# Performance work log

Hardware: AMD Instinct MI355X
Metric: run time of the kernel (lower is better)

## Reference

```python
import jax, jax.numpy as jnp
import numpy as np

B, S, DIM, HEADS, HEAD_DIM = 2, 1536, 1024, 16, 64
BLOCK_SIZE, LOOK_AHEAD, LOOK_BACKWARD = 24, 1, 1
ROPE_THETA = 10000.0


def setup_inputs() -> dict:
    key = jax.random.key(0)
    ks = jax.random.split(key, 6)
    s = 0.02  # init scale for weights
    return {
        "x": jax.random.normal(ks[0], (B, S, DIM), jnp.float32),
        "Wq": jax.random.normal(ks[1], (DIM, DIM), jnp.float32) * s,
        "bq": jnp.zeros((DIM,), jnp.float32),
        "Wk": jax.random.normal(ks[2], (DIM, DIM), jnp.float32) * s,
        "bk": jnp.zeros((DIM,), jnp.float32),
        "Wv": jax.random.normal(ks[3], (DIM, DIM), jnp.float32) * s,
        "bv": jnp.zeros((DIM,), jnp.float32),
        "Wo": jax.random.normal(ks[4], (DIM, DIM), jnp.float32) * s,
        "bo": jnp.zeros((DIM,), jnp.float32),
        "position_ids": jnp.arange(S, dtype=jnp.int32),
    }


def _rotate_half(v):
    # pairs (x1, x2) -> (-x2, x1), interleaved (matches torch reshape/unbind/stack)
    v2 = v.reshape(*v.shape[:-1], -1, 2)
    x1, x2 = v2[..., 0], v2[..., 1]
    return jnp.stack((-x2, x1), axis=-1).reshape(v.shape)


def _rope_tables(position_ids):
    # DitRotary: theta_i = 1/ROPE_THETA^(2i/rotary_dim), i=0..31; cos/sin duplicated
    # pairwise -> [c0,c0,c1,c1,...] of length HEAD_DIM
    inv_freq = 1.0 / (ROPE_THETA ** (jnp.arange(0, HEAD_DIM, 2, dtype=jnp.float32) / HEAD_DIM))
    ang = position_ids.astype(jnp.float32)[:, None] * inv_freq[None, :]  # [S, 32]
    cos = jnp.repeat(jnp.cos(ang), 2, axis=-1)  # [S, HEAD_DIM]
    sin = jnp.repeat(jnp.sin(ang), 2, axis=-1)
    return cos, sin


def reference(x, Wq, bq, Wk, bk, Wv, bv, Wo, bo, position_ids):
    b, s, _ = x.shape
    q = (x @ Wq + bq).reshape(b, s, HEADS, HEAD_DIM)
    k = (x @ Wk + bk).reshape(b, s, HEADS, HEAD_DIM)
    v = (x @ Wv + bv).reshape(b, s, HEADS, HEAD_DIM)

    # Partial rotary: applied ONLY to head 0 (torch slices dim=2 == heads)
    cos, sin = _rope_tables(position_ids)            # [S, HEAD_DIM]
    q0 = q[:, :, 0, :] * cos + _rotate_half(q[:, :, 0, :]) * sin
    k0 = k[:, :, 0, :] * cos + _rotate_half(k[:, :, 0, :]) * sin
    q = jnp.concatenate([q0[:, :, None, :], q[:, :, 1:, :]], axis=2)
    k = jnp.concatenate([k0[:, :, None, :], k[:, :, 1:, :]], axis=2)

    # Block-banded mask: diff[i, j] = block(j) - block(i)
    blk = position_ids // BLOCK_SIZE
    diff = blk[None, :] - blk[:, None]               # [S, S]
    allowed = (diff >= -LOOK_BACKWARD) & (diff <= LOOK_AHEAD)
    neg = jnp.where(allowed, 0.0, jnp.finfo(jnp.float32).min)  # ~mask * finfo.min

    scale = 1.0 / jnp.sqrt(jnp.float32(HEAD_DIM))
    scores = jnp.einsum("bqhd,bkhd->bhqk", q, k) * scale + neg[None, None]
    attn = jax.nn.softmax(scores.astype(jnp.float32), axis=-1).astype(q.dtype)
    out = jnp.einsum("bhqk,bkhd->bqhd", attn, v).reshape(b, s, HEADS * HEAD_DIM)
    return out @ Wo + bo
```

## Files before the change

kernel.cpp:

```cpp
#include <hip/hip_runtime.h>
#include <hip/hip_bf16.h>
#include <stdint.h>

typedef _Float16 f16;
typedef _Float16 f16x8 __attribute__((ext_vector_type(8)));
typedef float    f32x4 __attribute__((ext_vector_type(4)));
typedef unsigned short u16;
typedef unsigned int   u32;

#define S_LEN 1536
#define NDIM  1024
#define MROWS 3072

__device__ __forceinline__ u16 f2h(float f){
  _Float16 h = (_Float16)f;
  return __builtin_bit_cast(u16, h);
}

#define GLDS16(g, l) __builtin_amdgcn_global_load_lds( \
    (const __attribute__((address_space(1))) u32*)(const void*)(g), \
    (__attribute__((address_space(3))) u32*)(void*)(l), 16, 0, 0)

__global__ __launch_bounds__(256) void cast_f32_f16(
    const float* __restrict__ in, u16* __restrict__ out)
{
  const int i = blockIdx.x * 256 + threadIdx.x;
  const float4* p = (const float4*)in;
  float4 a = p[i*2], b = p[i*2+1];
  alignas(16) u16 tmp[8];
  tmp[0]=f2h(a.x); tmp[1]=f2h(a.y); tmp[2]=f2h(a.z); tmp[3]=f2h(a.w);
  tmp[4]=f2h(b.x); tmp[5]=f2h(b.y); tmp[6]=f2h(b.z); tmp[7]=f2h(b.w);
  *(uint4*)(out + (size_t)i*8) = *(const uint4*)tmp;
}

__global__ __launch_bounds__(256) void transpose4(
    const float* __restrict__ w0, const float* __restrict__ w1,
    const float* __restrict__ w2, const float* __restrict__ w3,
    u16* __restrict__ out)
{
  const float* W = (blockIdx.z==0)?w0:(blockIdx.z==1)?w1:(blockIdx.z==2)?w2:w3;
  u16* O = out + (size_t)blockIdx.z * (1024u*1024u);
  __shared__ __align__(16) u16 T[64*72];
  const int t = threadIdx.x;
  const int r0 = blockIdx.y*64, c0 = blockIdx.x*64;
  #pragma unroll
  for (int i=0;i<2;i++){
    int v = t + i*256;
    int row = v >> 3, col = (v & 7) * 8;
    const float* src = W + (size_t)(r0+row)*NDIM + c0 + col;
    float4 a = *(const float4*)src;
    float4 b = *(const float4*)(src + 4);
    alignas(16) u16 tmp[8];
    tmp[0]=f2h(a.x); tmp[1]=f2h(a.y); tmp[2]=f2h(a.z); tmp[3]=f2h(a.w);
    tmp[4]=f2h(b.x); tmp[5]=f2h(b.y); tmp[6]=f2h(b.z); tmp[7]=f2h(b.w);
    *(uint4*)(T + row*72 + col) = *(const uint4*)tmp;
  }
  __syncthreads();
  #pragma unroll
  for (int i=0;i<2;i++){
    int v = t + i*256;
    int cc = v >> 3, rr = (v & 7) * 8;
    alignas(16) u16 tmp[8];
    #pragma unroll
    for (int j=0;j<8;j++) tmp[j] = T[(rr+j)*72 + cc];
    *(uint4*)(O + (size_t)(c0+cc)*NDIM + r0 + rr) = *(const uint4*)tmp;
  }
}

#define SUBK 32

__global__ __launch_bounds__(256) void gemm_bias_rope(
    const u16* __restrict__ A,
    const u16* __restrict__ BT,
    const float* __restrict__ b0, const float* __restrict__ b1,
    const float* __restrict__ b2,
    u16*   __restrict__ Ch,
    float* __restrict__ Cf,
    const int* __restrict__ pos,
    int M, int rope_mats, int f32_out)
{
  __shared__ __align__(16) u16 As[2*128*SUBK];
  __shared__ __align__(16) u16 Bs[2*64*SUBK];

  const int t    = threadIdx.x;
  const int lane = t & 63;
  const int wave = t >> 6;
  const int z    = blockIdx.z;
  const int m0   = blockIdx.y * 128;
  const int n0   = blockIdx.x * 64;
  const u16* Bm  = BT + (size_t)z * (1024u*1024u);
  u16*       Cm  = Ch ? (Ch + (size_t)z * ((size_t)M * NDIM)) : (u16*)0;
  const float* bias = (z==0) ? b0 : ((z==1) ? b1 : b2);

  const int wm   = (wave >> 1) * 64;
  const int wn   = (wave & 1) * 32;
  const int l15  = lane & 15;
  const int quad = lane >> 4;

  const int lrow = lane >> 2;
  const int lcol = (lane & 3) * 8;
  const u16* gA = A  + (size_t)(m0 + wave*32 + lrow)*NDIM + lcol;
  const u16* gB = Bm + (size_t)(n0 + wave*16 + lrow)*NDIM + lcol;
  u16* lA = As + (wave*32)*SUBK;
  u16* lB = Bs + (wave*16)*SUBK;

  f32x4 acc[4][2];
  #pragma unroll
  for (int i=0;i<4;i++)
    #pragma unroll
    for (int j=0;j<2;j++)
      acc[i][j] = (f32x4){0.f,0.f,0.f,0.f};

  for (int k0 = 0; k0 < 1024; k0 += 64) {
    #pragma unroll
    for (int kb=0;kb<2;kb++){
      const u16* ga = gA + k0 + kb*SUBK;
      u16* la = lA + kb*(128*SUBK);
      GLDS16(ga,           la);
      GLDS16(ga + 16*NDIM, la + 16*SUBK);
      GLDS16(gB + k0 + kb*SUBK, lB + kb*(64*SUBK));
    }
    __syncthreads();
    #pragma unroll
    for (int kb=0;kb<2;kb++){
      f16x8 af[4], bfr[2];
      #pragma unroll
      for (int i=0;i<4;i++)
        af[i]  = *(const f16x8*)(As + kb*(128*SUBK) + (wm + i*16 + l15)*SUBK + quad*8);
      #pragma unroll
      for (int j=0;j<2;j++)
        bfr[j] = *(const f16x8*)(Bs + kb*(64*SUBK)  + (wn + j*16 + l15)*SUBK + quad*8);
      #pragma unroll
      for (int i=0;i<4;i++)
        #pragma unroll
        for (int j=0;j<2;j++)
          acc[i][j] = __builtin_amdgcn_mfma_f32_16x16x32_f16(
                          af[i], bfr[j], acc[i][j], 0, 0, 0);
    }
    __syncthreads();
  }

  const bool rope_tile = (z < rope_mats) && (n0 == 0);
  #pragma unroll
  for (int i=0;i<4;i++){
    const int rbase = m0 + wm + i*16 + quad*4;
    #pragma unroll
    for (int j=0;j<2;j++){
      const int c  = n0 + wn + j*16 + l15;
      const float bv = bias[c];
      f32x4 v4 = acc[i][j];
      #pragma unroll
      for (int r=0;r<4;r++) v4[r] += bv;
      if (rope_tile) {
        const int   ii  = c >> 1;
        const float inv = powf(10000.0f, -(float)ii * (1.0f/32.0f));
        const float sgn = (c & 1) ? 1.0f : -1.0f;
        #pragma unroll
        for (int r=0;r<4;r++){
          float val     = v4[r];
          float partner = __shfl_xor(val, 1, 64);
          int   srow    = (rbase + r) % S_LEN;
          float ang     = (float)pos[srow] * inv;
          float sv, cv;
          sincosf(ang, &sv, &cv);
          v4[r] = val * cv + sgn * partner * sv;
        }
      }
      if (f32_out) {
        #pragma unroll
        for (int r=0;r<4;r++)
          Cf[(size_t)(rbase + r)*NDIM + c] = v4[r];
      } else {
        #pragma unroll
        for (int r=0;r<4;r++)
          Cm[(size_t)(rbase + r)*NDIM + c] = f2h(v4[r]);
      }
    }
  }
}

__global__ __launch_bounds__(256) void attn_kernel(
    const u16* __restrict__ q, const u16* __restrict__ k,
    const u16* __restrict__ v, u16* __restrict__ o)
{
  const int qb = blockIdx.x;
  const int h  = blockIdx.y;
  const int b  = blockIdx.z;
  const int t  = threadIdx.x;
  const int lane = t & 63;
  const int wave = t >> 6;
  const int l15  = lane & 15;
  const int quad = lane >> 4;

  const int ks_ = (qb == 0) ? 0 : (qb - 1) * 24;
  const int ke_ = min(S_LEN, (qb + 2) * 24);
  const int kn  = ke_ - ks_;

  __shared__ __align__(16) u16   Qs[32*72];
  __shared__ __align__(16) u16   Ks[80*72];
  __shared__ __align__(16) u16   Vt[64*104];
  __shared__ __align__(16) float Ss[32*80];
  __shared__ __align__(16) u16   Ps[32*104];

  const size_t qrow0 = (size_t)b*S_LEN + qb*24;
  const size_t krow0 = (size_t)b*S_LEN + ks_;
  const int hoff = h * 64;

  if (t < 192) {
    int row = t >> 3, col = (t & 7) * 8;
    *(uint4*)(Qs + row*72 + col) = *(const uint4*)(q + (qrow0+row)*NDIM + hoff + col);
  }
  for (int e = t; e < kn*8; e += 256) {
    int row = e >> 3, col = (e & 7) * 8;
    *(uint4*)(Ks + row*72 + col) = *(const uint4*)(k + (krow0+row)*NDIM + hoff + col);
    uint4 vv = *(const uint4*)(v + (krow0+row)*NDIM + hoff + col);
    const u16* pu = (const u16*)&vv;
    #pragma unroll
    for (int j=0;j<8;j++) Vt[(col+j)*104 + row] = pu[j];
  }
  for (int e = t; e < 64*48; e += 256) {
    int d = e / 48, c = 48 + (e - (e/48)*48);
    if (c >= kn) Vt[d*104 + c] = 0;
  }
  __syncthreads();

  const int ntn = (kn + 15) >> 4;
  for (int id = wave; id < 2*ntn; id += 4) {
    int mt = id / ntn, nt = id - (id/ntn)*ntn;
    f32x4 acc = (f32x4){0.f,0.f,0.f,0.f};
    #pragma unroll
    for (int ks2 = 0; ks2 < 2; ks2++) {
      f16x8 a = *(const f16x8*)(Qs + (mt*16 + l15)*72 + ks2*32 + quad*8);
      f16x8 bb= *(const f16x8*)(Ks + (nt*16 + l15)*72 + ks2*32 + quad*8);
      acc = __builtin_amdgcn_mfma_f32_16x16x32_f16(a, bb, acc, 0, 0, 0);
    }
    #pragma unroll
    for (int r=0;r<4;r++)
      Ss[(mt*16 + quad*4 + r)*80 + nt*16 + l15] = acc[r] * 0.125f;
  }
  __syncthreads();

  #pragma unroll
  for (int i=0;i<6;i++){
    int row = wave*6 + i;
    float v0 = (lane      < kn) ? Ss[row*80 + lane]      : -1e30f;
    float v1 = (lane + 64 < kn) ? Ss[row*80 + 64 + lane] : -1e30f;
    float m = fmaxf(v0, v1);
    #pragma unroll
    for (int off=32; off; off>>=1) m = fmaxf(m, __shfl_xor(m, off, 64));
    float p0 = __expf(v0 - m);
    float p1 = __expf(v1 - m);
    float s = p0 + p1;
    #pragma unroll
    for (int off=32; off; off>>=1) s += __shfl_xor(s, off, 64);
    float inv = 1.0f / s;
    Ps[row*104 + lane] = f2h(p0 * inv);
    if (lane < 32) Ps[row*104 + 64 + lane] = f2h(p1 * inv);
  }
  __syncthreads();

  const int kceil = (kn + 31) >> 5;
  #pragma unroll
  for (int id2 = 0; id2 < 2; id2++){
    int id = wave*2 + id2;
    int mt = id >> 2, nt = id & 3;
    f32x4 acc = (f32x4){0.f,0.f,0.f,0.f};
    for (int ks2 = 0; ks2 < kceil; ks2++) {
      f16x8 a = *(const f16x8*)(Ps + (mt*16 + l15)*104 + ks2*32 + quad*8);
      f16x8 bb= *(const f16x8*)(Vt + (nt*16 + l15)*104 + ks2*32 + quad*8);
      acc = __builtin_amdgcn_mfma_f32_16x16x32_f16(a, bb, acc, 0, 0, 0);
    }
    #pragma unroll
    for (int r=0;r<4;r++){
      int row = mt*16 + quad*4 + r;
      if (row < 24)
        o[(qrow0 + row)*NDIM + hoff + nt*16 + l15] = f2h(acc[r]);
    }
  }
}

extern "C" void kernel_launch(void* const* d_in, const int* in_sizes, int n_in,
                              void* d_out, int out_size, void* d_ws, size_t ws_size,
                              hipStream_t stream)
{
  const float* x   = (const float*)d_in[0];
  const float* Wq  = (const float*)d_in[1];
  const float* bq  = (const float*)d_in[2];
  const float* Wk  = (const float*)d_in[3];
  const float* bk  = (const float*)d_in[4];
  const float* Wv  = (const float*)d_in[5];
  const float* bv  = (const float*)d_in[6];
  const float* Wo  = (const float*)d_in[7];
  const float* bo  = (const float*)d_in[8];
  const int*   pos = (const int*)d_in[9];

  u16* ws   = (u16*)d_ws;
  u16* WT   = ws;
  u16* xb   = WT + 4u*1024u*1024u;
  u16* qkv  = xb + (size_t)MROWS*NDIM;
  u16* attn = WT;
  float* outf = (float*)d_out;

  cast_f32_f16<<<dim3(MROWS*NDIM/(256*8)), 256, 0, stream>>>(x, xb);
  transpose4<<<dim3(16,16,4), 256, 0, stream>>>(Wq, Wk, Wv, Wo, WT);
  gemm_bias_rope<<<dim3(16,24,3), 256, 0, stream>>>(
      xb, WT, bq, bk, bv, qkv, nullptr, pos, MROWS, 2, 0);
  attn_kernel<<<dim3(64,16,2), 256, 0, stream>>>(
      qkv, qkv + (size_t)MROWS*NDIM, qkv + 2u*(size_t)MROWS*NDIM, attn);
  gemm_bias_rope<<<dim3(16,24,1), 256, 0, stream>>>(
      attn, WT + 3u*1024u*1024u, bo, bo, bo, nullptr, outf, pos, MROWS,
      0, 1);
}
```

Baseline: 179.9 us.

## Double-buffer GEMM LDS stages and use smaller M tile for output projection

The GEMM main loop now ping-pongs between two LDS buffers, so each next K-slice is issued with global_load_lds while MFMAs run on the current one, leaving one barrier per slice. The kernel is templated on the M tile size, and the output projection runs with a 64-row tile over twice as many blocks (768 instead of 384) to fill the GPU better. LDS use doubles for the 128-row variant, which may lower occupancy.

```diff
diff --git a/kernel.cpp b/kernel.cpp
--- a/kernel.cpp
+++ b/kernel.cpp
@@ -69,6 +69,7 @@
 
 #define SUBK 32
 
+template<int TM>
 __global__ __launch_bounds__(256) void gemm_bias_rope(
     const u16* __restrict__ A,
     const u16* __restrict__ BT,
@@ -79,70 +80,88 @@
     const int* __restrict__ pos,
     int M, int rope_mats, int f32_out)
 {
-  __shared__ __align__(16) u16 As[2*128*SUBK];
-  __shared__ __align__(16) u16 Bs[2*64*SUBK];
+  constexpr int TN   = 64;
+  constexpr int MI   = TM / 32;
+  constexpr int AW   = TM / 4;
+  constexpr int ABUF = TM * 64;
+  constexpr int BBUF = TN * 64;
+
+  __shared__ __align__(16) u16 As[2*ABUF];
+  __shared__ __align__(16) u16 Bs[2*BBUF];
 
   const int t    = threadIdx.x;
   const int lane = t & 63;
   const int wave = t >> 6;
   const int z    = blockIdx.z;
-  const int m0   = blockIdx.y * 128;
+  const int m0   = blockIdx.y * TM;
   const int n0   = blockIdx.x * 64;
   const u16* Bm  = BT + (size_t)z * (1024u*1024u);
   u16*       Cm  = Ch ? (Ch + (size_t)z * ((size_t)M * NDIM)) : (u16*)0;
   const float* bias = (z==0) ? b0 : ((z==1) ? b1 : b2);
 
-  const int wm   = (wave >> 1) * 64;
+  const int wm   = (wave >> 1) * (TM/2);
   const int wn   = (wave & 1) * 32;
   const int l15  = lane & 15;
   const int quad = lane >> 4;
 
   const int lrow = lane >> 2;
   const int lcol = (lane & 3) * 8;
-  const u16* gA = A  + (size_t)(m0 + wave*32 + lrow)*NDIM + lcol;
+  const u16* gA = A  + (size_t)(m0 + wave*AW + lrow)*NDIM + lcol;
   const u16* gB = Bm + (size_t)(n0 + wave*16 + lrow)*NDIM + lcol;
-  u16* lA = As + (wave*32)*SUBK;
-  u16* lB = Bs + (wave*16)*SUBK;
-
-  f32x4 acc[4][2];
-  #pragma unroll
-  for (int i=0;i<4;i++)
+
+  f32x4 acc[MI][2];
+  #pragma unroll
+  for (int i=0;i<MI;i++)
     #pragma unroll
     for (int j=0;j<2;j++)
       acc[i][j] = (f32x4){0.f,0.f,0.f,0.f};
 
-  for (int k0 = 0; k0 < 1024; k0 += 64) {
+  auto stage = [&](int k0, int buf) {
+    u16* la = As + buf*ABUF + (wave*AW)*SUBK;
+    u16* lb = Bs + buf*BBUF + (wave*16)*SUBK;
     #pragma unroll
     for (int kb=0;kb<2;kb++){
       const u16* ga = gA + k0 + kb*SUBK;
-      u16* la = lA + kb*(128*SUBK);
-      GLDS16(ga,           la);
-      GLDS16(ga + 16*NDIM, la + 16*SUBK);
-      GLDS16(gB + k0 + kb*SUBK, lB + kb*(64*SUBK));
-    }
-    __syncthreads();
+      u16* lak = la + kb*(TM*SUBK);
+      GLDS16(ga, lak);
+      if (TM == 128) GLDS16(ga + 16*NDIM, lak + 16*SUBK);
+      GLDS16(gB + k0 + kb*SUBK, lb + kb*(TN*SUBK));
+    }
+  };
+  auto compute = [&](int buf) {
     #pragma unroll
     for (int kb=0;kb<2;kb++){
-      f16x8 af[4], bfr[2];
+      f16x8 af[MI], bfr[2];
       #pragma unroll
-      for (int i=0;i<4;i++)
-        af[i]  = *(const f16x8*)(As + kb*(128*SUBK) + (wm + i*16 + l15)*SUBK + quad*8);
+      for (int i=0;i<MI;i++)
+        af[i]  = *(const f16x8*)(As + buf*ABUF + kb*(TM*SUBK)
+                                 + (wm + i*16 + l15)*SUBK + quad*8);
       #pragma unroll
       for (int j=0;j<2;j++)
-        bfr[j] = *(const f16x8*)(Bs + kb*(64*SUBK)  + (wn + j*16 + l15)*SUBK + quad*8);
+        bfr[j] = *(const f16x8*)(Bs + buf*BBUF + kb*(TN*SUBK)
+                                 + (wn + j*16 + l15)*SUBK + quad*8);
       #pragma unroll
-      for (int i=0;i<4;i++)
+      for (int i=0;i<MI;i++)
         #pragma unroll
         for (int j=0;j<2;j++)
           acc[i][j] = __builtin_amdgcn_mfma_f32_16x16x32_f16(
                           af[i], bfr[j], acc[i][j], 0, 0, 0);
     }
+  };
+
+  stage(0, 0);
+  for (int it = 0; it < 16; it += 2) {
     __syncthreads();
+    if (it + 1 < 16) stage((it+1)*64, 1);
+    compute(0);
+    __syncthreads();
+    if (it + 2 < 16) stage((it+2)*64, 0);
+    compute(1);
   }
 
   const bool rope_tile = (z < rope_mats) && (n0 == 0);
   #pragma unroll
-  for (int i=0;i<4;i++){
+  for (int i=0;i<MI;i++){
     const int rbase = m0 + wm + i*16 + quad*4;
     #pragma unroll
     for (int j=0;j<2;j++){
@@ -303,11 +322,11 @@
 
   cast_f32_f16<<<dim3(MROWS*NDIM/(256*8)), 256, 0, stream>>>(x, xb);
   transpose4<<<dim3(16,16,4), 256, 0, stream>>>(Wq, Wk, Wv, Wo, WT);
-  gemm_bias_rope<<<dim3(16,24,3), 256, 0, stream>>>(
+  gemm_bias_rope<128><<<dim3(16,24,3), 256, 0, stream>>>(
       xb, WT, bq, bk, bv, qkv, nullptr, pos, MROWS, 2, 0);
   attn_kernel<<<dim3(64,16,2), 256, 0, stream>>>(
       qkv, qkv + (size_t)MROWS*NDIM, qkv + 2u*(size_t)MROWS*NDIM, attn);
-  gemm_bias_rope<<<dim3(16,24,1), 256, 0, stream>>>(
+  gemm_bias_rope<64><<<dim3(16,48,1), 256, 0, stream>>>(
       attn, WT + 3u*1024u*1024u, bo, bo, bo, nullptr, outf, pos, MROWS,
       0, 1);
 }
```

New measurement: 185.7 us. 3.2% more time.
